# Optimization experiments

Hardware: AMD Instinct MI355X
Metric: run time of the kernel (lower is better)

Reference implementation:

```python
import jax, jax.numpy as jnp
import numpy as np

B_SZ, T, H, N, L = 4, 512, 256, 64, 4
EPS = 1e-5

def _hippo(n):
    i = np.arange(n)[:, None]; j = np.arange(n)[None, :]
    A = np.where(i >= j, ((-1.0) ** (i - j)) * np.sqrt((2 * i + 1.0) * (2 * j + 1.0)), 0.0)
    # scale to be contractive so the 512-step dense recurrence stays finite
    A = A / (1.1 * np.linalg.norm(A, 2))
    return A.astype(np.float32)

def _xavier(key, shape):
    fan_in, fan_out = shape[1], shape[0]
    a = float(np.sqrt(6.0 / (fan_in + fan_out)))
    return jax.random.uniform(key, shape, jnp.float32, -a, a)

def setup_inputs() -> dict:
    key = jax.random.key(0)
    ks = jax.random.split(key, 8)
    x = jax.random.normal(ks[0], (B_SZ, T, H), jnp.float32)
    A = jnp.broadcast_to(jnp.asarray(_hippo(N)), (L, N, N))
    Bm = jnp.stack([_xavier(jax.random.fold_in(ks[1], l), (N, H)) for l in range(L)])
    Cm = jnp.stack([_xavier(jax.random.fold_in(ks[2], l), (H, N)) for l in range(L)])
    Dm = jnp.stack([_xavier(jax.random.fold_in(ks[3], l), (H, H)) for l in range(L)])
    Win = _xavier(ks[4], (H, H)); bin_ = jnp.zeros((H,), jnp.float32)
    Wout = _xavier(ks[5], (H, H)); bout = jnp.zeros((H,), jnp.float32)
    return {"x": x, "Win": Win, "bin_": bin_, "Wout": Wout, "bout": bout,
            "A": A, "Bm": Bm, "Cm": Cm, "Dm": Dm}

def _ln(x):
    m = jnp.mean(x, -1, keepdims=True)
    v = jnp.mean((x - m) ** 2, -1, keepdims=True)
    return (x - m) / jnp.sqrt(v + EPS)

def _ssm_layer(h, A, B, C, D):
    # h: (B,T,H); dense state (B,N,H)
    Cbar = C.mean(0)            # mean over output rows (matches C_state.mean(dim=2))
    BT = B.T                    # (H,N)
    DT = D.T                    # (H,H)
    def step(state, u):        # state (B,N,H), u (B,H)
        y = jnp.einsum('bnh,n->bh', state, Cbar) + u @ DT   # output uses pre-update state
        new_state = jnp.einsum('nm,bmh->bnh', A, state) + (u @ BT)[:, :, None]
        return new_state, y
    state0 = jnp.zeros((h.shape[0], A.shape[0], h.shape[2]), h.dtype)
    _, ys = jax.lax.scan(step, state0, jnp.swapaxes(h, 0, 1))  # scan over T
    y = jnp.swapaxes(ys, 0, 1)
    y = jax.nn.gelu(y, approximate=False) + h   # GELU -> (dropout=0) -> residual
    return _ln(y)

def reference(x, Win, bin_, Wout, bout, A, Bm, Cm, Dm):
    h = x @ Win.T + bin_
    for l in range(L):
        h = _ssm_layer(h, A[l], Bm[l], Cm[l], Dm[l])
    h = _ln(h)
    return h @ Wout.T + bout
```

## Files before the change

### kernel.cpp

```cpp
#include <hip/hip_runtime.h>

#define TSEQ 512
#define HDIM 256
#define NDIM 64
#define LC   48
#define MT   16
#define NWB  128

typedef __attribute__((ext_vector_type(4))) float  f32x4;
typedef __attribute__((ext_vector_type(8))) short  s16x8;
typedef __attribute__((ext_vector_type(4))) unsigned short u16x4;
typedef unsigned long long u64;
typedef unsigned short us;

#define MFMA16 __builtin_amdgcn_mfma_f32_16x16x32_bf16

__device__ __forceinline__ float lane_bcast(float v, int l) {
    return __int_as_float(__builtin_amdgcn_readlane(__float_as_int(v), l));
}
__device__ __forceinline__ us f2bf(float f) {
    unsigned u = __float_as_uint(f);
    u += 0x7fffu + ((u >> 16) & 1u);
    return (us)(u >> 16);
}
__device__ __forceinline__ float bf2f(us h) {
    return __uint_as_float(((unsigned)h) << 16);
}
__device__ __forceinline__ int swz(int row, int chunk) {
    return row * 512 + (((chunk) ^ (row & 7)) << 4);
}
__device__ __forceinline__ void st_mall(float* p, float v) {
    __hip_atomic_store(p, v, __ATOMIC_RELAXED, __HIP_MEMORY_SCOPE_AGENT);
}
__device__ __forceinline__ u64 ld_mall8(const u64* p) {
    return __hip_atomic_load(p, __ATOMIC_RELAXED, __HIP_MEMORY_SCOPE_AGENT);
}
__device__ __forceinline__ void flag_set(unsigned* f) {
    __hip_atomic_store(f, 1u, __ATOMIC_RELAXED, __HIP_MEMORY_SCOPE_AGENT);
}
__device__ __forceinline__ void flag_wait(const unsigned* f) {
    while (__hip_atomic_load(f, __ATOMIC_RELAXED, __HIP_MEMORY_SCOPE_AGENT) == 0u)
        __builtin_amdgcn_s_sleep(4);
}

__global__ void __launch_bounds__(256) k_prep(
    const float* __restrict__ Win, const float* __restrict__ Wout,
    const float* __restrict__ Bm, const float* __restrict__ Dm,
    const float* __restrict__ Cm, const float* __restrict__ A,
    us* __restrict__ Win_bf, us* __restrict__ Wout_bf,
    us* __restrict__ Bm_bf, us* __restrict__ Dm_bf,
    float* __restrict__ cbar_g, float* __restrict__ wA8,
    unsigned* __restrict__ flags)
{
    __shared__ __align__(16) float Pa[4096];
    __shared__ __align__(16) float Pb[4096];
    const int gid = blockIdx.x, tid = threadIdx.x;

    if (gid < 128) {
        for (int q = gid * 256 + tid; q < 114688; q += 32768) {
            const float* s; us* d; int off;
            if (q < 16384)      { s = Win;  d = Win_bf;  off = q; }
            else if (q < 32768) { s = Wout; d = Wout_bf; off = q - 16384; }
            else if (q < 49152) { s = Bm;   d = Bm_bf;   off = q - 32768; }
            else                { s = Dm;   d = Dm_bf;   off = q - 49152; }
            f32x4 v = ((const f32x4*)s)[off];
            u16x4 p; p[0] = f2bf(v[0]); p[1] = f2bf(v[1]); p[2] = f2bf(v[2]); p[3] = f2bf(v[3]);
            ((u16x4*)d)[off] = p;
        }
        return;
    }
    if (gid == 128) {
        for (int i = tid; i < 4 + 4 * NWB; i += 256)
            __hip_atomic_store(&flags[i], 0u, __ATOMIC_RELAXED, __HIP_MEMORY_SCOPE_AGENT);
        const int l = tid >> 6, n = tid & 63;
        const float* cp = Cm + (size_t)l * HDIM * NDIM + n;
        float s0 = 0.f, s1 = 0.f, s2 = 0.f, s3 = 0.f;
        for (int h = 0; h < HDIM; h += 4) {
            s0 += cp[(h + 0) * NDIM]; s1 += cp[(h + 1) * NDIM];
            s2 += cp[(h + 2) * NDIM]; s3 += cp[(h + 3) * NDIM];
        }
        cbar_g[tid] = ((s0 + s1) + (s2 + s3)) * (1.0f / HDIM);
        return;
    }
    for (int q = tid; q < 1024; q += 256) ((f32x4*)Pa)[q] = ((const f32x4*)A)[q];
    __syncthreads();
    const int r0 = (tid >> 3) * 2, c0 = (tid & 7) * 8;
    const f32x4 z4 = {0.f, 0.f, 0.f, 0.f};
#pragma unroll 1
    for (int it = 0; it < 3; ++it) {
        const float* S = (it & 1) ? Pb : Pa;
        float*       D = (it & 1) ? Pa : Pb;
        f32x4 s00 = z4, s01 = z4, s10 = z4, s11 = z4;
        for (int k = 0; k < 64; ++k) {
            float a0 = S[r0 * 64 + k], a1 = S[(r0 + 1) * 64 + k];
            f32x4 b0 = *(const f32x4*)(S + k * 64 + c0);
            f32x4 b1 = *(const f32x4*)(S + k * 64 + c0 + 4);
            s00 += a0 * b0; s01 += a0 * b1; s10 += a1 * b0; s11 += a1 * b1;
        }
        *(f32x4*)(D + r0 * 64 + c0) = s00;       *(f32x4*)(D + r0 * 64 + c0 + 4) = s01;
        *(f32x4*)(D + (r0 + 1) * 64 + c0) = s10; *(f32x4*)(D + (r0 + 1) * 64 + c0 + 4) = s11;
        __syncthreads();
    }
    for (int q = tid; q < 1024; q += 256) ((f32x4*)wA8)[q] = ((const f32x4*)Pb)[q];
}

__global__ void __launch_bounds__(512, 2) k_fused(
    const float* __restrict__ x, const float* __restrict__ bin,
    const float* __restrict__ bout, const float* __restrict__ A,
    const float* __restrict__ wA8, const float* __restrict__ cbar_g,
    const us* __restrict__ Win_bf, const us* __restrict__ Wout_bf,
    const us* __restrict__ Bm_bf, const us* __restrict__ Dm_bf,
    float* __restrict__ wbuf, float* __restrict__ BiA, float* __restrict__ BiB,
    unsigned* __restrict__ flags, float* __restrict__ out)
{
    __shared__ __align__(16) char smem[53568];
    us*    xl   = (us*)smem;
    float* yl   = (float*)(smem + 8192);
    float* bwin = (float*)(smem + 24832);
    float* wlds = (float*)(smem + 41216);
    float* cfin = (float*)(smem + 53504);

    const int gid = blockIdx.x, tid = threadIdx.x;
    const int lane = tid & 63, wv = tid >> 6;
    const int m = lane & 15, cgq = lane >> 4;
    const f32x4 z4 = {0.f, 0.f, 0.f, 0.f};

    if (gid == NWB) {
        float* As  = (float*)smem;
        float* A8s = (float*)(smem + 16384);
        float* uls = (float*)(smem + 32768);
        for (int q = tid; q < 1024; q += 512) {
            ((f32x4*)As)[q]  = ((const f32x4*)A)[q];
            ((f32x4*)A8s)[q] = ((const f32x4*)wA8)[q];
        }
        __syncthreads();
        if (wv < 4) {
            const int l = wv;
            float u = cbar_g[l * 64 + lane];
            uls[(l * 8 + 0) * 64 + lane] = u;
#pragma unroll 1
            for (int s = 1; s < 8; ++s) {
                float p0 = 0.f, p1 = 0.f, p2 = 0.f, p3 = 0.f;
#pragma unroll
                for (int k = 0; k < 64; k += 4) {
                    p0 += As[(k + 0) * 64 + lane] * lane_bcast(u, k + 0);
                    p1 += As[(k + 1) * 64 + lane] * lane_bcast(u, k + 1);
                    p2 += As[(k + 2) * 64 + lane] * lane_bcast(u, k + 2);
                    p3 += As[(k + 3) * 64 + lane] * lane_bcast(u, k + 3);
                }
                u = (p0 + p1) + (p2 + p3);
                uls[(l * 8 + s) * 64 + lane] = u;
            }
        }
        __syncthreads();
        {
            const int p = wv;
            float u = uls[p * 64 + lane];
#pragma unroll 1
            for (int k6 = 0; k6 < 6; ++k6) {
                st_mall(&wbuf[(size_t)(p + 8 * k6) * 64 + lane], u);
                if (k6 < 5) {
                    float n0 = 0.f;
#pragma unroll
                    for (int k = 0; k < 64; ++k)
                        n0 += A8s[k * 64 + lane] * lane_bcast(u, k);
                    u = n0;
                }
            }
        }
        __syncthreads();
        if (tid == 0) flag_set(&flags[0]);
        {
            const int p = wv;
            float u1 = uls[(8 + p) * 64 + lane];
            float u2 = uls[(16 + p) * 64 + lane];
            float u3 = uls[(24 + p) * 64 + lane];
#pragma unroll 1
            for (int k6 = 0; k6 < 6; ++k6) {
                const int j = p + 8 * k6;
                st_mall(&wbuf[(size_t)(1 * LC + j) * 64 + lane], u1);
                st_mall(&wbuf[(size_t)(2 * LC + j) * 64 + lane], u2);
                st_mall(&wbuf[(size_t)(3 * LC + j) * 64 + lane], u3);
                if (k6 < 5) {
                    float n1 = 0.f, n2 = 0.f, n3 = 0.f;
#pragma unroll
                    for (int k = 0; k < 64; ++k) {
                        float a = A8s[k * 64 + lane];
                        n1 += a * lane_bcast(u1, k); n2 += a * lane_bcast(u2, k);
                        n3 += a * lane_bcast(u3, k);
                    }
                    u1 = n1; u2 = n2; u3 = n3;
                }
            }
        }
        __syncthreads();
        if (tid < 3) flag_set(&flags[1 + tid]);
        return;
    }

    const int b = gid >> 5, tb = gid & 31, t0 = tb * MT;
    const size_t grow = (size_t)(b * TSEQ + t0);

    {
        const f32x4* gs = (const f32x4*)(x + grow * HDIM);
#pragma unroll
        for (int k = 0; k < 2; ++k) {
            int q = tid + k * 512;
            int row = q >> 6, c4 = q & 63;
            f32x4 v = gs[q];
            u16x4 pk; pk[0] = f2bf(v[0]); pk[1] = f2bf(v[1]); pk[2] = f2bf(v[2]); pk[3] = f2bf(v[3]);
            *(u16x4*)((char*)xl + swz(row, c4 >> 1) + (c4 & 1) * 8) = pk;
        }
    }
    __syncthreads();

    {
        f32x4 accA = z4, accB = z4;
        const us* W0 = Win_bf + (size_t)(wv * 32 + m) * HDIM;
        const us* W1 = W0 + (size_t)16 * HDIM;
#pragma unroll
        for (int ks = 0; ks < 8; ++ks) {
            s16x8 av = *(const s16x8*)((const char*)xl + swz(m, ks * 4 + cgq));
            s16x8 b0 = *(const s16x8*)(W0 + ks * 32 + cgq * 8);
            s16x8 b1 = *(const s16x8*)(W1 + ks * 32 + cgq * 8);
            accA = MFMA16(av, b0, accA, 0, 0, 0);
            accB = MFMA16(av, b1, accB, 0, 0, 0);
        }
        __syncthreads();
        const int h0c = wv * 32 + m, h1c = h0c + 16;
        float bi0 = bin[h0c], bi1 = bin[h1c];
#pragma unroll
        for (int reg = 0; reg < 4; ++reg) {
            int trow = cgq * 4 + reg;
            *(us*)((char*)xl + swz(trow, h0c >> 3) + (h0c & 7) * 2) = f2bf(accA[reg] + bi0);
            *(us*)((char*)xl + swz(trow, h1c >> 3) + (h1c & 7) * 2) = f2bf(accB[reg] + bi1);
        }
    }
    __syncthreads();

    if (wv < 4) {
        f32x4 accb = z4;
        const us* B0 = Bm_bf + (size_t)(wv * 16 + m) * HDIM;
#pragma unroll
        for (int ks = 0; ks < 8; ++ks) {
            s16x8 av = *(const s16x8*)((const char*)xl + swz(m, ks * 4 + cgq));
            s16x8 bv = *(const s16x8*)(B0 + ks * 32 + cgq * 8);
            accb = MFMA16(av, bv, accb, 0, 0, 0);
        }
#pragma unroll
        for (int reg = 0; reg < 4; ++reg)
            st_mall(&BiA[(grow + cgq * 4 + reg) * NDIM + wv * 16 + m], accb[reg]);
    }
    __syncthreads();
    if (tid == 0) flag_set(&flags[4 + 0 * NWB + gid]);

#pragma unroll 1
    for (int l = 0; l < 4; ++l) {
        const us* Dl = Dm_bf + (size_t)l * HDIM * HDIM;
        const float* bi = (l & 1) ? BiB : BiA;
        float*       bo = (l & 1) ? BiA : BiB;

        f32x4 accA = z4, accB = z4;
        {
            const us* D0 = Dl + (size_t)(wv * 32 + m) * HDIM;
            const us* D1 = D0 + (size_t)16 * HDIM;
#pragma unroll
            for (int ks = 0; ks < 8; ++ks) {
                s16x8 av = *(const s16x8*)((const char*)xl + swz(m, ks * 4 + cgq));
                s16x8 b0 = *(const s16x8*)(D0 + ks * 32 + cgq * 8);
                s16x8 b1 = *(const s16x8*)(D1 + ks * 32 + cgq * 8);
                accA = MFMA16(av, b0, accA, 0, 0, 0);
                accB = MFMA16(av, b1, accB, 0, 0, 0);
            }
        }

        if (tid == 0) {
            flag_wait(&flags[l]);
#pragma unroll
            for (int nb = 1; nb <= 3; ++nb)
                if (tb - nb >= 0) flag_wait(&flags[4 + l * NWB + gid - nb]);
        }
        __syncthreads();

        {
            const u64* ws8 = (const u64*)(wbuf + (size_t)l * LC * NDIM);
            for (int q = tid; q < LC * NDIM / 2; q += 512)
                ((u64*)wlds)[q] = ld_mall8(&ws8[q]);
            const u64* bi8 = (const u64*)(bi + (size_t)b * TSEQ * NDIM);
#pragma unroll
            for (int k = 0; k < 4; ++k) {
                int q = tid + k * 512;
                int r = q >> 5, cc = q & 31;
                int t = t0 - LC + r;
                ((u64*)bwin)[q] = (t >= 0) ? ld_mall8(&bi8[(size_t)t * 32 + cc]) : 0ull;
            }
        }
        __syncthreads();

        {
            const int r0 = wv * 2;
            float c0 = 0.f, c1 = 0.f;
            float v0 = bwin[(LC - 1 + r0) * NDIM + lane];
            float v1 = bwin[(LC + r0) * NDIM + lane];
#pragma unroll
            for (int j = 0; j < LC; ++j) {
                float wj = wlds[j * NDIM + lane];
                c0 += wj * v0; c1 += wj * v1;
                v1 = v0;
                int nr = LC - 2 + r0 - j; nr = nr < 0 ? 0 : nr;
                v0 = bwin[nr * NDIM + lane];
            }
#pragma unroll
            for (int k = 1; k < 64; k <<= 1) {
                c0 += __shfl_xor(c0, k, 64); c1 += __shfl_xor(c1, k, 64);
            }
            if (lane == 0) { cfin[r0] = c0; cfin[r0 + 1] = c1; }
        }
        __syncthreads();

#pragma unroll
        for (int nt = 0; nt < 2; ++nt) {
            int hcol = wv * 32 + nt * 16 + m;
#pragma unroll
            for (int reg = 0; reg < 4; ++reg) {
                int trow = cgq * 4 + reg;
                float val = (nt ? accB[reg] : accA[reg]) + cfin[trow];
                float g = 0.5f * val * (1.0f + erff(val * 0.70710678118654752f));
                float r = bf2f(*(const us*)((const char*)xl + swz(trow, hcol >> 3) + (hcol & 7) * 2));
                yl[trow * 260 + hcol] = g + r;
            }
        }
        __syncthreads();

        {
            const bool last = (l == 3);
#pragma unroll
            for (int q = 0; q < 2; ++q) {
                int r = wv * 2 + q;
                f32x4 yv = *(const f32x4*)(yl + r * 260 + lane * 4);
                float s = (yv[0] + yv[1]) + (yv[2] + yv[3]);
                float sq = yv[0] * yv[0] + yv[1] * yv[1] + yv[2] * yv[2] + yv[3] * yv[3];
#pragma unroll
                for (int k = 1; k < 64; k <<= 1) {
                    s += __shfl_xor(s, k, 64); sq += __shfl_xor(sq, k, 64);
                }
                float mn = s * (1.0f / HDIM);
                float var = sq * (1.0f / HDIM) - mn * mn;
                float rs = rsqrtf(var + 1e-5f);
                if (last) { float vz = var * rs * rs; rs = rs * rsqrtf(vz + 1e-5f); }
                u16x4 zp;
                zp[0] = f2bf((yv[0] - mn) * rs); zp[1] = f2bf((yv[1] - mn) * rs);
                zp[2] = f2bf((yv[2] - mn) * rs); zp[3] = f2bf((yv[3] - mn) * rs);
                *(u16x4*)((char*)xl + swz(r, lane >> 1) + (lane & 1) * 8) = zp;
            }
        }
        __syncthreads();

        if (l < 3) {
            if (wv < 4) {
                f32x4 accb = z4;
                const us* B0 = Bm_bf + (size_t)(l + 1) * NDIM * HDIM + (size_t)(wv * 16 + m) * HDIM;
#pragma unroll
                for (int ks = 0; ks < 8; ++ks) {
                    s16x8 av = *(const s16x8*)((const char*)xl + swz(m, ks * 4 + cgq));
                    s16x8 bv = *(const s16x8*)(B0 + ks * 32 + cgq * 8);
                    accb = MFMA16(av, bv, accb, 0, 0, 0);
                }
#pragma unroll
                for (int reg = 0; reg < 4; ++reg)
                    st_mall(&bo[(grow + cgq * 4 + reg) * NDIM + wv * 16 + m], accb[reg]);
            }
            __syncthreads();
            if (tid == 0) flag_set(&flags[4 + (l + 1) * NWB + gid]);
        } else {
            f32x4 a2A = z4, a2B = z4;
            const us* W0 = Wout_bf + (size_t)(wv * 32 + m) * HDIM;
            const us* W1 = W0 + (size_t)16 * HDIM;
#pragma unroll
            for (int ks = 0; ks < 8; ++ks) {
                s16x8 av = *(const s16x8*)((const char*)xl + swz(m, ks * 4 + cgq));
                s16x8 b0 = *(const s16x8*)(W0 + ks * 32 + cgq * 8);
                s16x8 b1 = *(const s16x8*)(W1 + ks * 32 + cgq * 8);
                a2A = MFMA16(av, b0, a2A, 0, 0, 0);
                a2B = MFMA16(av, b1, a2B, 0, 0, 0);
            }
#pragma unroll
            for (int nt = 0; nt < 2; ++nt) {
                int hcol = wv * 32 + nt * 16 + m;
                float bo2 = bout[hcol];
#pragma unroll
                for (int reg = 0; reg < 4; ++reg) {
                    int trow = cgq * 4 + reg;
                    out[(grow + trow) * HDIM + hcol] = (nt ? a2B[reg] : a2A[reg]) + bo2;
                }
            }
        }
    }
}

extern "C" void kernel_launch(void* const* d_in, const int* in_sizes, int n_in,
                              void* d_out, int out_size, void* d_ws, size_t ws_size,
                              hipStream_t stream) {
    (void)in_sizes; (void)n_in; (void)out_size; (void)ws_size;
    const float* x    = (const float*)d_in[0];
    const float* Win  = (const float*)d_in[1];
    const float* bin  = (const float*)d_in[2];
    const float* Wout = (const float*)d_in[3];
    const float* bout = (const float*)d_in[4];
    const float* A    = (const float*)d_in[5];
    const float* Bm   = (const float*)d_in[6];
    const float* Cm   = (const float*)d_in[7];
    const float* Dm   = (const float*)d_in[8];

    float* ws     = (float*)d_ws;
    float* wbuf   = ws;
    float* cbar_g = ws + 16384;
    float* wA8    = ws + 17408;
    float* biA    = ws + 21504;
    float* biB    = ws + 152576;
    unsigned* flags = (unsigned*)(ws + 283648);
    us* Win_bf  = (us*)(ws + 284672);
    us* Wout_bf = Win_bf + 65536;
    us* Bm_bf   = Wout_bf + 65536;
    us* Dm_bf   = Bm_bf + 65536;
    float* out  = (float*)d_out;

    k_prep<<<130, 256, 0, stream>>>(Win, Wout, Bm, Dm, Cm, A,
                                    Win_bf, Wout_bf, Bm_bf, Dm_bf, cbar_g, wA8, flags);
    k_fused<<<NWB + 1, 512, 0, stream>>>(x, bin, bout, A, wA8, cbar_g,
                                         Win_bf, Wout_bf, Bm_bf, Dm_bf,
                                         wbuf, biA, biB, flags, out);
}
```

Before: 67.46 us.

## Fold prep kernel into fused kernel with in-kernel grid barrier

Removes the separate prep kernel launch. The bf16 weight conversion is now spread across the 128 worker blocks, followed by a global atomic counter barrier. The Cbar reduction and the A^8 matrix power are computed inside the special producer block, and a memset replaces the flag-reset kernel work. This cuts one kernel launch and its serialization, at the cost of a spin barrier across all blocks, which requires all blocks to be co-resident, plus extra serial work on the producer block.

```diff
diff --git a/kernel.cpp b/kernel.cpp
--- a/kernel.cpp
+++ b/kernel.cpp
@@ -32,6 +32,9 @@
 __device__ __forceinline__ void st_mall(float* p, float v) {
     __hip_atomic_store(p, v, __ATOMIC_RELAXED, __HIP_MEMORY_SCOPE_AGENT);
 }
+__device__ __forceinline__ void st_mall8(u64* p, u64 v) {
+    __hip_atomic_store(p, v, __ATOMIC_RELAXED, __HIP_MEMORY_SCOPE_AGENT);
+}
 __device__ __forceinline__ u64 ld_mall8(const u64* p) {
     return __hip_atomic_load(p, __ATOMIC_RELAXED, __HIP_MEMORY_SCOPE_AGENT);
 }
@@ -43,73 +46,14 @@
         __builtin_amdgcn_s_sleep(4);
 }
 
-__global__ void __launch_bounds__(256) k_prep(
-    const float* __restrict__ Win, const float* __restrict__ Wout,
-    const float* __restrict__ Bm, const float* __restrict__ Dm,
-    const float* __restrict__ Cm, const float* __restrict__ A,
-    us* __restrict__ Win_bf, us* __restrict__ Wout_bf,
-    us* __restrict__ Bm_bf, us* __restrict__ Dm_bf,
-    float* __restrict__ cbar_g, float* __restrict__ wA8,
-    unsigned* __restrict__ flags)
-{
-    __shared__ __align__(16) float Pa[4096];
-    __shared__ __align__(16) float Pb[4096];
-    const int gid = blockIdx.x, tid = threadIdx.x;
-
-    if (gid < 128) {
-        for (int q = gid * 256 + tid; q < 114688; q += 32768) {
-            const float* s; us* d; int off;
-            if (q < 16384)      { s = Win;  d = Win_bf;  off = q; }
-            else if (q < 32768) { s = Wout; d = Wout_bf; off = q - 16384; }
-            else if (q < 49152) { s = Bm;   d = Bm_bf;   off = q - 32768; }
-            else                { s = Dm;   d = Dm_bf;   off = q - 49152; }
-            f32x4 v = ((const f32x4*)s)[off];
-            u16x4 p; p[0] = f2bf(v[0]); p[1] = f2bf(v[1]); p[2] = f2bf(v[2]); p[3] = f2bf(v[3]);
-            ((u16x4*)d)[off] = p;
-        }
-        return;
-    }
-    if (gid == 128) {
-        for (int i = tid; i < 4 + 4 * NWB; i += 256)
-            __hip_atomic_store(&flags[i], 0u, __ATOMIC_RELAXED, __HIP_MEMORY_SCOPE_AGENT);
-        const int l = tid >> 6, n = tid & 63;
-        const float* cp = Cm + (size_t)l * HDIM * NDIM + n;
-        float s0 = 0.f, s1 = 0.f, s2 = 0.f, s3 = 0.f;
-        for (int h = 0; h < HDIM; h += 4) {
-            s0 += cp[(h + 0) * NDIM]; s1 += cp[(h + 1) * NDIM];
-            s2 += cp[(h + 2) * NDIM]; s3 += cp[(h + 3) * NDIM];
-        }
-        cbar_g[tid] = ((s0 + s1) + (s2 + s3)) * (1.0f / HDIM);
-        return;
-    }
-    for (int q = tid; q < 1024; q += 256) ((f32x4*)Pa)[q] = ((const f32x4*)A)[q];
-    __syncthreads();
-    const int r0 = (tid >> 3) * 2, c0 = (tid & 7) * 8;
-    const f32x4 z4 = {0.f, 0.f, 0.f, 0.f};
-#pragma unroll 1
-    for (int it = 0; it < 3; ++it) {
-        const float* S = (it & 1) ? Pb : Pa;
-        float*       D = (it & 1) ? Pa : Pb;
-        f32x4 s00 = z4, s01 = z4, s10 = z4, s11 = z4;
-        for (int k = 0; k < 64; ++k) {
-            float a0 = S[r0 * 64 + k], a1 = S[(r0 + 1) * 64 + k];
-            f32x4 b0 = *(const f32x4*)(S + k * 64 + c0);
-            f32x4 b1 = *(const f32x4*)(S + k * 64 + c0 + 4);
-            s00 += a0 * b0; s01 += a0 * b1; s10 += a1 * b0; s11 += a1 * b1;
-        }
-        *(f32x4*)(D + r0 * 64 + c0) = s00;       *(f32x4*)(D + r0 * 64 + c0 + 4) = s01;
-        *(f32x4*)(D + (r0 + 1) * 64 + c0) = s10; *(f32x4*)(D + (r0 + 1) * 64 + c0 + 4) = s11;
-        __syncthreads();
-    }
-    for (int q = tid; q < 1024; q += 256) ((f32x4*)wA8)[q] = ((const f32x4*)Pb)[q];
-}
-
 __global__ void __launch_bounds__(512, 2) k_fused(
     const float* __restrict__ x, const float* __restrict__ bin,
     const float* __restrict__ bout, const float* __restrict__ A,
-    const float* __restrict__ wA8, const float* __restrict__ cbar_g,
-    const us* __restrict__ Win_bf, const us* __restrict__ Wout_bf,
-    const us* __restrict__ Bm_bf, const us* __restrict__ Dm_bf,
+    const float* __restrict__ Bm, const float* __restrict__ Cm,
+    const float* __restrict__ Dm, const float* __restrict__ Win,
+    const float* __restrict__ Wout,
+    us* __restrict__ Win_bf, us* __restrict__ Wout_bf,
+    us* __restrict__ Bm_bf, us* __restrict__ Dm_bf,
     float* __restrict__ wbuf, float* __restrict__ BiA, float* __restrict__ BiB,
     unsigned* __restrict__ flags, float* __restrict__ out)
 {
@@ -124,20 +68,29 @@
     const int lane = tid & 63, wv = tid >> 6;
     const int m = lane & 15, cgq = lane >> 4;
     const f32x4 z4 = {0.f, 0.f, 0.f, 0.f};
+    unsigned* ctr = &flags[516];
 
     if (gid == NWB) {
         float* As  = (float*)smem;
         float* A8s = (float*)(smem + 16384);
         float* uls = (float*)(smem + 32768);
-        for (int q = tid; q < 1024; q += 512) {
-            ((f32x4*)As)[q]  = ((const f32x4*)A)[q];
-            ((f32x4*)A8s)[q] = ((const f32x4*)wA8)[q];
-        }
-        __syncthreads();
+        float cbv = 0.f;
         if (wv < 4) {
-            const int l = wv;
-            float u = cbar_g[l * 64 + lane];
-            uls[(l * 8 + 0) * 64 + lane] = u;
+            const float* cp = Cm + (size_t)wv * HDIM * NDIM + lane;
+            float s0 = 0.f, s1 = 0.f, s2 = 0.f, s3 = 0.f;
+            for (int h = 0; h < HDIM; h += 4) {
+                s0 += cp[(h + 0) * NDIM]; s1 += cp[(h + 1) * NDIM];
+                s2 += cp[(h + 2) * NDIM]; s3 += cp[(h + 3) * NDIM];
+            }
+            cbv = ((s0 + s1) + (s2 + s3)) * (1.0f / HDIM);
+        } else {
+            int t = tid - 256;
+            for (int q = t; q < 1024; q += 256) ((f32x4*)As)[q] = ((const f32x4*)A)[q];
+        }
+        __syncthreads();
+        if (wv < 4) {
+            float u = cbv;
+            uls[(wv * 8 + 0) * 64 + lane] = u;
 #pragma unroll 1
             for (int s = 1; s < 8; ++s) {
                 float p0 = 0.f, p1 = 0.f, p2 = 0.f, p3 = 0.f;
@@ -149,16 +102,52 @@
                     p3 += As[(k + 3) * 64 + lane] * lane_bcast(u, k + 3);
                 }
                 u = (p0 + p1) + (p2 + p3);
-                uls[(l * 8 + s) * 64 + lane] = u;
-            }
-        }
-        __syncthreads();
-        {
-            const int p = wv;
-            float u = uls[p * 64 + lane];
+                uls[(wv * 8 + s) * 64 + lane] = u;
+            }
+        } else {
+            int t = tid - 256;
+            int r = t >> 2, c0 = (t & 3) * 16;
+            f32x4 a0 = z4, a1 = z4, a2 = z4, a3 = z4;
+            for (int k = 0; k < 64; ++k) {
+                float av = As[r * 64 + k];
+                const f32x4* bp = (const f32x4*)(As + k * 64 + c0);
+                a0 += av * bp[0]; a1 += av * bp[1]; a2 += av * bp[2]; a3 += av * bp[3];
+            }
+            f32x4* dp = (f32x4*)(A8s + r * 64 + c0);
+            dp[0] = a0; dp[1] = a1; dp[2] = a2; dp[3] = a3;
+        }
+        __syncthreads();
+        {
+            int r = tid >> 3, c0 = (tid & 7) * 8;
+            f32x4 a0 = z4, a1 = z4;
+            for (int k = 0; k < 64; ++k) {
+                float av = A8s[r * 64 + k];
+                const f32x4* bp = (const f32x4*)(A8s + k * 64 + c0);
+                a0 += av * bp[0]; a1 += av * bp[1];
+            }
+            __syncthreads();
+            *(f32x4*)(As + r * 64 + c0) = a0;
+            *(f32x4*)(As + r * 64 + c0 + 4) = a1;
+        }
+        __syncthreads();
+        {
+            int r = tid >> 3, c0 = (tid & 7) * 8;
+            f32x4 a0 = z4, a1 = z4;
+            for (int k = 0; k < 64; ++k) {
+                float av = As[r * 64 + k];
+                const f32x4* bp = (const f32x4*)(As + k * 64 + c0);
+                a0 += av * bp[0]; a1 += av * bp[1];
+            }
+            __syncthreads();
+            *(f32x4*)(A8s + r * 64 + c0) = a0;
+            *(f32x4*)(A8s + r * 64 + c0 + 4) = a1;
+        }
+        __syncthreads();
+        {
+            float u = uls[wv * 64 + lane];
 #pragma unroll 1
             for (int k6 = 0; k6 < 6; ++k6) {
-                st_mall(&wbuf[(size_t)(p + 8 * k6) * 64 + lane], u);
+                st_mall(&wbuf[(size_t)(wv + 8 * k6) * 64 + lane], u);
                 if (k6 < 5) {
                     float n0 = 0.f;
 #pragma unroll
@@ -171,13 +160,12 @@
         __syncthreads();
         if (tid == 0) flag_set(&flags[0]);
         {
-            const int p = wv;
-            float u1 = uls[(8 + p) * 64 + lane];
-            float u2 = uls[(16 + p) * 64 + lane];
-            float u3 = uls[(24 + p) * 64 + lane];
+            float u1 = uls[(8 + wv) * 64 + lane];
+            float u2 = uls[(16 + wv) * 64 + lane];
+            float u3 = uls[(24 + wv) * 64 + lane];
 #pragma unroll 1
             for (int k6 = 0; k6 < 6; ++k6) {
-                const int j = p + 8 * k6;
+                const int j = wv + 8 * k6;
                 st_mall(&wbuf[(size_t)(1 * LC + j) * 64 + lane], u1);
                 st_mall(&wbuf[(size_t)(2 * LC + j) * 64 + lane], u2);
                 st_mall(&wbuf[(size_t)(3 * LC + j) * 64 + lane], u3);
@@ -202,6 +190,20 @@
     const size_t grow = (size_t)(b * TSEQ + t0);
 
     {
+        const int base = gid * 896;
+        for (int q = base + tid; q < base + 896; q += 512) {
+            const float* s; us* d; int off;
+            if (q < 16384)      { s = Win;  d = Win_bf;  off = q; }
+            else if (q < 32768) { s = Wout; d = Wout_bf; off = q - 16384; }
+            else if (q < 49152) { s = Bm;   d = Bm_bf;   off = q - 32768; }
+            else                { s = Dm;   d = Dm_bf;   off = q - 49152; }
+            f32x4 v = ((const f32x4*)s)[off];
+            u64 pk = (u64)f2bf(v[0]) | ((u64)f2bf(v[1]) << 16)
+                   | ((u64)f2bf(v[2]) << 32) | ((u64)f2bf(v[3]) << 48);
+            st_mall8((u64*)d + off, pk);
+        }
+    }
+    {
         const f32x4* gs = (const f32x4*)(x + grow * HDIM);
 #pragma unroll
         for (int k = 0; k < 2; ++k) {
@@ -211,6 +213,12 @@
             u16x4 pk; pk[0] = f2bf(v[0]); pk[1] = f2bf(v[1]); pk[2] = f2bf(v[2]); pk[3] = f2bf(v[3]);
             *(u16x4*)((char*)xl + swz(row, c4 >> 1) + (c4 & 1) * 8) = pk;
         }
+    }
+    __syncthreads();
+    if (tid == 0) {
+        __hip_atomic_fetch_add(ctr, 1u, __ATOMIC_RELAXED, __HIP_MEMORY_SCOPE_AGENT);
+        while (__hip_atomic_load(ctr, __ATOMIC_RELAXED, __HIP_MEMORY_SCOPE_AGENT) < 128u)
+            __builtin_amdgcn_s_sleep(4);
     }
     __syncthreads();
 
@@ -414,8 +422,6 @@
 
     float* ws     = (float*)d_ws;
     float* wbuf   = ws;
-    float* cbar_g = ws + 16384;
-    float* wA8    = ws + 17408;
     float* biA    = ws + 21504;
     float* biB    = ws + 152576;
     unsigned* flags = (unsigned*)(ws + 283648);
@@ -425,9 +431,8 @@
     us* Dm_bf   = Bm_bf + 65536;
     float* out  = (float*)d_out;
 
-    k_prep<<<130, 256, 0, stream>>>(Win, Wout, Bm, Dm, Cm, A,
-                                    Win_bf, Wout_bf, Bm_bf, Dm_bf, cbar_g, wA8, flags);
-    k_fused<<<NWB + 1, 512, 0, stream>>>(x, bin, bout, A, wA8, cbar_g,
+    hipMemsetAsync(flags, 0, 520 * sizeof(unsigned), stream);
+    k_fused<<<NWB + 1, 512, 0, stream>>>(x, bin, bout, A, Bm, Cm, Dm, Win, Wout,
                                          Win_bf, Wout_bf, Bm_bf, Dm_bf,
                                          wbuf, biA, biB, flags, out);
 }
```

After: 71.74 us. 1.06x slower.
